# Optimization experiments

Hardware: AMD Instinct MI355X
Metric: run time of the kernel (lower is better)

The kernel has to match this reference:

```python
import jax, jax.numpy as jnp
import numpy as np
import math

B, S, L, K, NSTEPS = 32, 128, 4096, 129, 10
PAD = K // 2  # torch: int(kernel.shape[-1]/2)


def _grouped_xcorr(x, w):
    # torch F.conv1d semantics (cross-correlation), groups = channels
    # x: [B,C,L] f32, w: [C,1,K] f32 -> [B,C,L]
    return jax.lax.conv_general_dilated(
        x, w, window_strides=(1,), padding=[(PAD, PAD)],
        dimension_numbers=('NCH', 'OIH', 'NCH'), feature_group_count=x.shape[1])


def _matched_filter(x_re, x_im, k_re, k_im):
    # complex grouped conv with conj(kernel) repeated per pulse
    wc_re = jnp.tile(k_re[None, None, :], (S, 1, 1))
    wc_im = jnp.tile(-k_im[None, None, :], (S, 1, 1))  # conj
    out_re = _grouped_xcorr(x_re, wc_re) - _grouped_xcorr(x_im, wc_im)
    out_im = _grouped_xcorr(x_re, wc_im) + _grouped_xcorr(x_im, wc_re)
    return out_re + 1j * out_im  # complex64 [B,S,L]


def _produce_rd(x, w_mag, w_phase):
    phase = jnp.arctan(w_phase)                    # [B,S]
    norm_mag = S * jax.nn.softmax(w_mag, axis=-1)  # [B,S]
    iq = (norm_mag * jnp.exp(-1j * phase))[..., None] * x
    return jnp.fft.fftshift(jnp.fft.fft(iq, axis=-2), axes=-2)


def _circular_weighted_mean(w):
    # circular weighted mean of index over last axis; returns (magnitude, index)
    N = w.shape[-1]
    ang = (2.0 * jnp.pi / N) * jnp.arange(N, dtype=w.dtype)
    z = jnp.sum(w * jnp.exp(1j * ang), axis=-1)
    return jnp.abs(z), jnp.angle(z) / (2.0 * jnp.pi) * N


def _snr(rd):
    Bn, nfft, Ln = rd.shape
    e = jnp.abs(rd) ** 2                                   # [B,S,L]
    flat_idx = jnp.argmax(e.reshape(Bn, -1), axis=1)
    max_range = flat_idx % Ln                              # [B] (indices: constant wrt grad)
    col = jnp.take_along_axis(e, max_range[:, None, None], axis=2)[..., 0]  # [B,S]
    _, peak_idx = _circular_weighted_mean(col)
    # torch rounds + casts to int -> detached index
    idx = jax.lax.stop_gradient(jnp.round(peak_idx)).astype(jnp.int32) % nfft
    peak = jnp.take_along_axis(col, idx[:, None], axis=1)[:, 0]
    noise = (jnp.sum(col, axis=-1) - peak) / (nfft - 1)
    return 10.0 * jnp.log10(peak) - 10.0 * jnp.log10(noise)


def setup_inputs() -> dict:
    key = jax.random.key(0)
    ks = jax.random.split(key, 5)
    return {
        'x_re': jax.random.normal(ks[0], (B, S, L), jnp.float32),
        'x_im': jax.random.normal(ks[1], (B, S, L), jnp.float32),
        'kernel_re': jax.random.normal(ks[2], (K,), jnp.float32),
        'kernel_im': jax.random.normal(ks[3], (K,), jnp.float32),
        'log_step_mag': -2.0 * jnp.ones((S, NSTEPS), jnp.float32),
        'log_step_phase': -2.0 * jnp.ones((S, NSTEPS), jnp.float32),
        'w_phase_init': jax.random.uniform(ks[4], (B, S), jnp.float32),
    }


def reference(x_re, x_im, kernel_re, kernel_im, log_step_mag, log_step_phase, w_phase_init):
    x = _matched_filter(x_re, x_im, kernel_re, kernel_im)  # [B,S,L] complex64
    w_mag = jnp.ones((B, S), jnp.float32)
    w_phase = w_phase_init

    def loss_sum(wm, wp):
        return jnp.sum(_snr(_produce_rd(x, wm, wp)))

    grad_fn = jax.grad(loss_sum, argnums=(0, 1))
    ln10 = math.log(10.0)
    for i in range(NSTEPS):
        # torch detaches w_mag/w_phase before the inner autograd.grad
        g_mag, g_phase = grad_fn(jax.lax.stop_gradient(w_mag),
                                 jax.lax.stop_gradient(w_phase))
        lr_mag = jnp.exp(log_step_mag[:, i] * ln10)    # 10**log_step
        lr_phase = jnp.exp(log_step_phase[:, i] * ln10)
        w_mag = w_mag + lr_mag * g_mag
        w_phase = w_phase + lr_phase * g_phase
    return jnp.mean(_snr(_produce_rd(x, w_mag, w_phase)))
```

## Files before the change

kernel.cpp:

```cpp
#include <hip/hip_runtime.h>

#define BB 32
#define SS 128
#define LL 4096
#define KK 129
#define NST 10

typedef float v2f __attribute__((ext_vector_type(2)));

constexpr double PI_D = 3.141592653589793238462643383279502884;
constexpr double red_sin(double x){
  double x2 = x*x, t = x, r = x;
  t *= -x2/6.0;   r += t;
  t *= -x2/20.0;  r += t;
  t *= -x2/42.0;  r += t;
  t *= -x2/72.0;  r += t;
  t *= -x2/110.0; r += t;
  t *= -x2/156.0; r += t;
  t *= -x2/210.0; r += t;
  t *= -x2/272.0; r += t;
  return r;
}
constexpr double csin_d(double x){
  while (x >  PI_D) x -= 2.0*PI_D;
  while (x < -PI_D) x += 2.0*PI_D;
  if (x >  PI_D*0.5)      x =  PI_D - x;
  else if (x < -PI_D*0.5) x = -PI_D - x;
  return red_sin(x);
}
constexpr double ccos_d(double x){ return csin_d(x + PI_D*0.5); }
struct TWT { float c[64]; float s[64]; };
constexpr TWT make_tw(){
  TWT t{};
  for (int j = 0; j < 64; j++){
    double a = -2.0*PI_D*(double)j/128.0;
    t.c[j] = (float)ccos_d(a);
    t.s[j] = (float)csin_d(a);
  }
  return t;
}
constexpr TWT TW = make_tw();

#define PHYS8(i) ((i) + ((i) >> 3))

__device__ __forceinline__ void cfma_pk(v2f& acc, v2f xv, v2f w){
  asm("v_pk_fma_f32 %0, %1, %2, %0 op_sel:[0,0,0] op_sel_hi:[1,0,1]"
      : "+v"(acc) : "v"(xv), "v"(w));
  asm("v_pk_fma_f32 %0, %1, %2, %0 op_sel:[1,1,0] op_sel_hi:[0,1,1] neg_hi:[1,0,0]"
      : "+v"(acc) : "v"(xv), "v"(w));
}

__global__ __launch_bounds__(256) void mf_kernel(const float* __restrict__ xr,
                                                 const float* __restrict__ xi,
                                                 const float* __restrict__ kr,
                                                 const float* __restrict__ ki,
                                                 float2* __restrict__ out)
{
  const int row = blockIdx.x >> 1;
  const int l0  = (blockIdx.x & 1) * 2048;
  const int t   = threadIdx.x;
  __shared__ float2 xs[2456];

  const float* xrr = xr + (size_t)row*LL;
  const float* xir = xi + (size_t)row*LL;
  for (int i4 = t; i4 < 544; i4 += 256){
    const int g0 = l0 - 64 + i4*4;
    float4 a, c;
    if (g0 >= 0 && g0 + 3 < LL){
      a = *(const float4*)(xrr + g0);
      c = *(const float4*)(xir + g0);
    } else {
      float av[4], cv[4];
      #pragma unroll
      for (int e = 0; e < 4; ++e){
        const int g = g0 + e;
        const bool ok = (g >= 0 && g < LL);
        av[e] = ok ? xrr[g] : 0.0f;
        cv[e] = ok ? xir[g] : 0.0f;
      }
      a = make_float4(av[0],av[1],av[2],av[3]);
      c = make_float4(cv[0],cv[1],cv[2],cv[3]);
    }
    const int i = i4*4;
    const int p = PHYS8(i);
    xs[p]   = make_float2(a.x, c.x);
    xs[p+1] = make_float2(a.y, c.y);
    xs[p+2] = make_float2(a.z, c.z);
    xs[p+3] = make_float2(a.w, c.w);
  }
  __syncthreads();

  const int base_l = t*8;
  v2f ring[16];
  #pragma unroll
  for (int v = 0; v < 12; v += 2){
    const float4 p = *(const float4*)(&xs[PHYS8(base_l + v)]);
    ring[v]   = (v2f){p.x, p.y};
    ring[v+1] = (v2f){p.z, p.w};
  }

  v2f acc[8];
  #pragma unroll
  for (int j = 0; j < 8; j++) acc[j] = (v2f){0.0f, 0.0f};

  #pragma unroll 1
  for (int q8 = 0; q8 < 8; ++q8){
    #pragma unroll
    for (int qq = 0; qq < 4; ++qq){
      const int q = q8*4 + qq;
      float4 p0, p1;
      const bool doref = (q < 31);
      if (doref){
        const int v0 = base_l + q*4 + 12;
        p0 = *(const float4*)(&xs[PHYS8(v0)]);
        p1 = *(const float4*)(&xs[PHYS8(v0 + 2)]);
      }
      #pragma unroll
      for (int kk = 0; kk < 4; ++kk){
        const v2f w = (v2f){ kr[q*4 + kk], ki[q*4 + kk] };
        #pragma unroll
        for (int j = 0; j < 8; ++j){
          const int sl = (qq*4 + kk + j) & 15;
          cfma_pk(acc[j], ring[sl], w);
        }
      }
      if (doref){
        const int s0 = (qq*4 + 12) & 15;
        ring[s0]   = (v2f){p0.x, p0.y};
        ring[s0+1] = (v2f){p0.z, p0.w};
        ring[s0+2] = (v2f){p1.x, p1.y};
        ring[s0+3] = (v2f){p1.z, p1.w};
      }
    }
  }
  {
    const v2f w = (v2f){ kr[128], ki[128] };
    #pragma unroll
    for (int j = 0; j < 8; ++j) cfma_pk(acc[j], ring[j], w);
  }

  float4* orow = (float4*)(out + (size_t)row*LL + l0 + base_l);
  #pragma unroll
  for (int q = 0; q < 4; ++q){
    orow[q] = make_float4(acc[2*q][0], acc[2*q][1], acc[2*q+1][0], acc[2*q+1][1]);
  }
}

__global__ void init_kernel(const float* __restrict__ wpi,
                            float* __restrict__ w_mag, float* __restrict__ w_phase,
                            float2* __restrict__ cvec, unsigned long long* __restrict__ slots,
                            float* __restrict__ out)
{
  const int i = blockIdx.x*256 + threadIdx.x;
  if (i < BB*SS){
    float wp = wpi[i];
    w_mag[i] = 1.0f;
    w_phase[i] = wp;
    float phi = atanf(wp);
    float s, c;
    sincosf(phi, &s, &c);
    cvec[i] = make_float2(c, -s);
  }
  if (i < BB) slots[i] = 0ull;
  if (i == 0) out[0] = 0.0f;
}

template<int SPAN, int N>
__device__ __forceinline__ void fstage(float2* v){
  #pragma unroll
  for (int b0 = 0; b0 < N; b0 += 2*SPAN){
    #pragma unroll
    for (int j = 0; j < SPAN; j++){
      const int i0 = b0 + j, i1 = b0 + j + SPAN;
      float ax = v[i0].x, ay = v[i0].y, bx = v[i1].x, by = v[i1].y;
      float sx = ax - bx, sy = ay - by;
      v[i0].x = ax + bx; v[i0].y = ay + by;
      const int tj = j * (64 / SPAN);
      if (tj == 0){
        v[i1].x = sx; v[i1].y = sy;
      } else if (tj == 32){
        v[i1].x = sy; v[i1].y = -sx;
      } else {
        const float wr = TW.c[tj], wi = TW.s[tj];
        v[i1].x = sx*wr - sy*wi;
        v[i1].y = sy*wr + sx*wi;
      }
    }
  }
}

__device__ __forceinline__ void scan_fft_tail(float2* v, int r, int tid, int l,
                                              unsigned long long* wred, int nwave,
                                              unsigned long long* slot)
{
  {
    const bool hi = (r & 2) != 0;
    const float sgn = hi ? -1.0f : 1.0f;
    const bool odd = (r & 1) != 0;
    #pragma unroll
    for (int j = 0; j < 32; ++j){
      float px = __shfl_xor(v[j].x, 2);
      float py = __shfl_xor(v[j].y, 2);
      float ux = fmaf(sgn, v[j].x, px);
      float uy = fmaf(sgn, v[j].y, py);
      float wr = hi ? (odd ? TW.s[j] : TW.c[j]) : 1.0f;
      float wi = hi ? (odd ? -TW.c[j] : TW.s[j]) : 0.0f;
      v[j].x = ux*wr - uy*wi;
      v[j].y = uy*wr + ux*wi;
    }
  }
  {
    const bool hi = (r & 1) != 0;
    const float sgn = hi ? -1.0f : 1.0f;
    #pragma unroll
    for (int j = 0; j < 32; ++j){
      float px = __shfl_xor(v[j].x, 1);
      float py = __shfl_xor(v[j].y, 1);
      float ux = fmaf(sgn, v[j].x, px);
      float uy = fmaf(sgn, v[j].y, py);
      float wr = hi ? TW.c[2*j] : 1.0f;
      float wi = hi ? TW.s[2*j] : 0.0f;
      v[j].x = ux*wr - uy*wi;
      v[j].y = uy*wr + ux*wi;
    }
  }
  fstage<16,32>(v); fstage<8,32>(v); fstage<4,32>(v); fstage<2,32>(v); fstage<1,32>(v);

  float mm = 0.0f;
  #pragma unroll
  for (int j = 0; j < 32; ++j) mm = fmaxf(mm, v[j].x*v[j].x + v[j].y*v[j].y);
  mm = fmaxf(mm, __shfl_xor(mm, 1));
  mm = fmaxf(mm, __shfl_xor(mm, 2));

  unsigned long long pk = ((unsigned long long)__float_as_uint(mm) << 32) | (unsigned int)l;
  #pragma unroll
  for (int m = 4; m < 64; m <<= 1){
    unsigned long long o = __shfl_xor(pk, m);
    if (o > pk) pk = o;
  }
  if ((tid & 63) == 0) wred[tid >> 6] = pk;
  __syncthreads();
  if (tid == 0){
    unsigned long long best = wred[0];
    for (int w = 1; w < nwave; ++w) if (wred[w] > best) best = wred[w];
    atomicMax(slot, best);
  }
}

__global__ __launch_bounds__(256) void tr_scan_kernel(const float2* __restrict__ xmf,
                                                      float4* __restrict__ xt2,
                                                      const float2* __restrict__ cvec,
                                                      unsigned long long* __restrict__ slots)
{
  const int b = blockIdx.y;
  const int l0 = blockIdx.x * 64;
  const int tid = threadIdx.x;
  __shared__ float ldr[SS][65];
  __shared__ float ldi[SS][65];
  __shared__ float2 csh[SS];
  __shared__ unsigned long long wred[4];
  if (tid < SS) csh[tid] = cvec[b*SS + tid];

  #pragma unroll
  for (int it = 0; it < 16; ++it){
    const int flat = it*256 + tid;
    const int s  = flat >> 5;
    const int c4 = flat & 31;
    const float4 p = *(const float4*)(xmf + ((size_t)(b*SS + s))*LL + l0 + 2*c4);
    const int sw = 8*(s >> 5);
    ldr[s][(2*c4   + sw) & 63] = p.x;  ldi[s][(2*c4   + sw) & 63] = p.y;
    ldr[s][(2*c4+1 + sw) & 63] = p.z;  ldi[s][(2*c4+1 + sw) & 63] = p.w;
  }
  __syncthreads();

  float4* dst = xt2 + ((size_t)(b*256 + blockIdx.x*4) * 16) * 64;
  #pragma unroll
  for (int it = 0; it < 16; ++it){
    const int flat = it*256 + tid;
    const int lane = flat & 63;
    const int i   = (flat >> 6) & 15;
    const int lgl = flat >> 10;
    const int fl = lane >> 2, rr = lane & 3;
    const int lrow = lgl*16 + fl;
    const int s0 = rr*32 + 2*i;
    const int col = (lrow + 8*rr) & 63;
    dst[flat] = make_float4(ldr[s0][col], ldi[s0][col], ldr[s0+1][col], ldi[s0+1][col]);
  }

  const int f = tid >> 2, r = tid & 3;
  const int l = l0 + f;
  float2 v[32];
  #pragma unroll
  for (int j = 0; j < 32; ++j){
    const int rowi = r*32 + j;
    const int col = (f + 8*r) & 63;
    const float2 x = make_float2(ldr[rowi][col], ldi[rowi][col]);
    const float2 c = csh[rowi];
    v[j].x = c.x*x.x - c.y*x.y;
    v[j].y = c.x*x.y + c.y*x.x;
  }
  scan_fft_tail(v, r, tid, l, wred, 4, slots + b);
}

__global__ __launch_bounds__(256) void scan_t_kernel(const float4* __restrict__ xt2,
                                                     const float2* __restrict__ cvec,
                                                     unsigned long long* __restrict__ slots)
{
  const int b = blockIdx.y;
  const int tid = threadIdx.x;
  const int f = tid >> 2, r = tid & 3;
  const int l = blockIdx.x*64 + f;
  const int w = tid >> 6;
  const int lg = blockIdx.x*4 + w;
  __shared__ float2 csh[SS];
  __shared__ unsigned long long wred[4];
  if (tid < SS) csh[tid] = cvec[b*SS + tid];
  __syncthreads();

  const float4* base = xt2 + ((size_t)(b*(LL/16) + lg) * 16) * 64 + (tid & 63);
  float2 v[32];
  #pragma unroll
  for (int i = 0; i < 16; ++i){
    const float4 p = base[i*64];
    v[2*i]   = make_float2(p.x, p.y);
    v[2*i+1] = make_float2(p.z, p.w);
  }
  #pragma unroll
  for (int j = 0; j < 32; ++j){
    const float2 c = csh[r*32 + j];
    const float2 x = v[j];
    v[j].x = c.x*x.x - c.y*x.y;
    v[j].y = c.x*x.y + c.y*x.x;
  }
  scan_fft_tail(v, r, tid, l, wred, 4, slots + b);
}

__global__ __launch_bounds__(512, 4) void scan_o_kernel(const float2* __restrict__ xmf,
                                                        const float2* __restrict__ cvec,
                                                        unsigned long long* __restrict__ slots)
{
  const int b = blockIdx.y;
  const int tid = threadIdx.x;
  const int l0 = blockIdx.x * 128;
  __shared__ float2 csh[SS];
  __shared__ float2 xsh[64][130];
  __shared__ unsigned long long wred[8];
  if (tid < SS) csh[tid] = cvec[b*SS + tid];

  const int f = tid >> 2, r = tid & 3;
  float2 v[32];

  #pragma unroll 1
  for (int h = 0; h < 2; ++h){
    __syncthreads();
    const float2* src = xmf + ((size_t)(b*SS + h*64))*LL + l0;
    #pragma unroll
    for (int it = 0; it < 8; ++it){
      const int flat = it*512 + tid;
      const int s1 = flat >> 6;
      const int c4 = flat & 63;
      const float4 vv = *(const float4*)(src + (size_t)s1*LL + c4*2);
      *(float4*)(&xsh[s1][c4*2]) = vv;
    }
    __syncthreads();
    if ((r >> 1) == h){
      #pragma unroll
      for (int j = 0; j < 32; ++j){
        const int rowi = (r & 1)*32 + j;
        const float2 x = xsh[rowi][f];
        const float2 c = csh[r*32 + j];
        v[j].x = c.x*x.x - c.y*x.y;
        v[j].y = c.x*x.y + c.y*x.x;
      }
    }
  }
  scan_fft_tail(v, r, tid, l0 + f, wred, 8, slots + b);
}

__device__ __forceinline__ float wredsum(float v){
  #pragma unroll
  for (int m = 1; m < 64; m <<= 1) v += __shfl_xor(v, m);
  return v;
}
__device__ __forceinline__ float wredmax(float v){
  #pragma unroll
  for (int m = 1; m < 64; m <<= 1) v = fmaxf(v, __shfl_xor(v, m));
  return v;
}
__device__ __forceinline__ float bsum256(float v, float* red4, int t){
  v = wredsum(v);
  __syncthreads();
  if ((t & 63) == 0) red4[t >> 6] = v;
  __syncthreads();
  return red4[0] + red4[1] + red4[2] + red4[3];
}
__device__ __forceinline__ float bmax256(float v, float* red4, int t){
  v = wredmax(v);
  __syncthreads();
  if ((t & 63) == 0) red4[t >> 6] = v;
  __syncthreads();
  return fmaxf(fmaxf(red4[0], red4[1]), fmaxf(red4[2], red4[3]));
}

__global__ __launch_bounds__(256) void step_kernel(const float2* __restrict__ xmf,
                                                   float* __restrict__ w_mag,
                                                   float* __restrict__ w_phase,
                                                   float2* __restrict__ cvec,
                                                   unsigned long long* __restrict__ slots,
                                                   const float* __restrict__ lsm,
                                                   const float* __restrict__ lsp,
                                                   int stepi, int isFinal,
                                                   float* __restrict__ out)
{
  const int b = blockIdx.x, t = threadIdx.x;
  const int s = t >> 1, h = t & 1;
  __shared__ float2 ysh[SS];
  __shared__ float twc[SS], tws[SS];
  __shared__ float red4[4];
  __shared__ float speak;
  __shared__ int sidx;

  const int rbin = (int)(slots[b] & 0xffffffffull);
  const float wm0 = w_mag[b*SS + s];
  const float wp0 = w_phase[b*SS + s];
  const float2 xc = xmf[((size_t)(b*SS + s))*LL + rbin];
  float phi = atanf(wp0);
  float sph, cph;
  sincosf(phi, &sph, &cph);
  {
    int id = t & 127;
    float sv, cv;
    sincosf((float)(2.0*PI_D/128.0) * (float)id, &sv, &cv);
    twc[id] = cv; tws[id] = -sv;
  }
  float mx = bmax256(wm0, red4, t);
  float ex = expf(wm0 - mx);
  float sm = bsum256(ex, red4, t) * 0.5f;
  float m = 128.0f * ex / sm;
  float cre = m*cph, cim = -m*sph;
  ysh[s] = make_float2(cre*xc.x - cim*xc.y, cre*xc.y + cim*xc.x);
  __syncthreads();

  const int k = s;
  float Fr = 0.0f, Fi = 0.0f;
  #pragma unroll 8
  for (int q = 0; q < 64; ++q){
    int s2 = h*64 + q;
    int id = (k*s2) & 127;
    float wr = twc[id], wi = tws[id];
    float2 ys = ysh[s2];
    Fr += wr*ys.x - wi*ys.y;
    Fi += wr*ys.y + wi*ys.x;
  }
  Fr += __shfl_xor(Fr, 1);
  Fi += __shfl_xor(Fi, 1);
  const int u = (k + 64) & 127;
  float colu = Fr*Fr + Fi*Fi;

  float total = bsum256(colu, red4, t) * 0.5f;
  float zre = bsum256(colu * twc[u], red4, t) * 0.5f;
  float zim = bsum256(colu * (-tws[u]), red4, t) * 0.5f;
  if (t == 0){
    float ang = atan2f(zim, zre);
    float pidx = ang * (128.0f/(2.0f*(float)PI_D));
    sidx = ((int)rintf(pidx)) & 127;
  }
  __syncthreads();
  const int idx = sidx;
  if (u == idx && h == 0) speak = colu;
  __syncthreads();
  const float peak = speak;
  const float noise = (total - peak) * (1.0f/127.0f);

  if (isFinal){
    if (t == 0) atomicAdd(out, 10.0f*(log10f(peak) - log10f(noise)) * (1.0f/(float)BB));
    return;
  }

  constexpr float C10 = 4.342944819032518f;
  float g = (u == idx) ? (C10/peak) : (-C10/(127.0f*noise));
  __syncthreads();
  ysh[k] = make_float2(2.0f*g*Fr, 2.0f*g*Fi);
  __syncthreads();

  float Tr = 0.0f, Ti = 0.0f;
  #pragma unroll 8
  for (int q = 0; q < 64; ++q){
    int kk = h*64 + q;
    int id = (s*kk) & 127;
    float wr = twc[id], wi = -tws[id];
    float2 G = ysh[kk];
    Tr += wr*G.x - wi*G.y;
    Ti += wr*G.y + wi*G.x;
  }
  Tr += __shfl_xor(Tr, 1);
  Ti += __shfl_xor(Ti, 1);

  float Hr = xc.x*Tr + xc.y*Ti;
  float Hi = xc.x*Ti - xc.y*Tr;
  float dm   = Hr*cph - Hi*sph;
  float dphi = -m*(Hr*sph + Hi*cph);
  float S1 = bsum256(m*dm, red4, t) * 0.5f;
  float gwm = m*(dm - S1*(1.0f/128.0f));
  float gwp = dphi / (1.0f + wp0*wp0);

  constexpr float LN10 = 2.302585092994046f;
  float lrm = expf(lsm[s*NST + stepi] * LN10);
  float lrp = expf(lsp[s*NST + stepi] * LN10);
  float wm1 = wm0 + lrm*gwm;
  float wp1 = wp0 + lrp*gwp;
  if (h == 0){
    w_mag[b*SS + s] = wm1;
    w_phase[b*SS + s] = wp1;
  }

  float mx2 = bmax256(wm1, red4, t);
  float ex2 = expf(wm1 - mx2);
  float sm2 = bsum256(ex2, red4, t) * 0.5f;
  float m2 = 128.0f * ex2 / sm2;
  float phi2 = atanf(wp1);
  float s2v, c2v;
  sincosf(phi2, &s2v, &c2v);
  if (h == 0) cvec[b*SS + s] = make_float2(m2*c2v, -m2*s2v);
  if (t == 0) slots[b] = 0ull;
}

extern "C" void kernel_launch(void* const* d_in, const int* in_sizes, int n_in,
                              void* d_out, int out_size, void* d_ws, size_t ws_size,
                              hipStream_t stream)
{
  const float* x_re = (const float*)d_in[0];
  const float* x_im = (const float*)d_in[1];
  const float* k_re = (const float*)d_in[2];
  const float* k_im = (const float*)d_in[3];
  const float* lsm  = (const float*)d_in[4];
  const float* lsp  = (const float*)d_in[5];
  const float* wpi  = (const float*)d_in[6];
  float* out = (float*)d_out;

  char* ws = (char*)d_ws;
  size_t off = 0;
  float2* xmf = (float2*)(ws + off);                 off += (size_t)BB*SS*LL*sizeof(float2);
  unsigned long long* slots = (unsigned long long*)(ws + off); off += 256;
  float* w_mag   = (float*)(ws + off);               off += (size_t)BB*SS*4;
  float* w_phase = (float*)(ws + off);               off += (size_t)BB*SS*4;
  float2* cvec   = (float2*)(ws + off);              off += (size_t)BB*SS*8;
  const size_t off_base = off;
  float4* xt2 = (float4*)(ws + off);                 off += (size_t)BB*SS*LL*sizeof(float2);
  const int useT = (ws_size >= off) ? 1 : 0;
  if (ws_size < off_base) return;

  mf_kernel<<<BB*SS*2, 256, 0, stream>>>(x_re, x_im, k_re, k_im, xmf);
  init_kernel<<<(BB*SS + 255)/256, 256, 0, stream>>>(wpi, w_mag, w_phase, cvec, slots, out);

  if (useT){
    tr_scan_kernel<<<dim3(LL/64, BB), 256, 0, stream>>>(xmf, xt2, cvec, slots);
    step_kernel<<<BB, 256, 0, stream>>>(xmf, w_mag, w_phase, cvec, slots, lsm, lsp, 0, 0, out);
    for (int i = 1; i < NST; i++){
      scan_t_kernel<<<dim3(LL/64, BB), 256, 0, stream>>>(xt2, cvec, slots);
      step_kernel<<<BB, 256, 0, stream>>>(xmf, w_mag, w_phase, cvec, slots, lsm, lsp, i, 0, out);
    }
    scan_t_kernel<<<dim3(LL/64, BB), 256, 0, stream>>>(xt2, cvec, slots);
    step_kernel<<<BB, 256, 0, stream>>>(xmf, w_mag, w_phase, cvec, slots, lsm, lsp, 0, 1, out);
  } else {
    for (int i = 0; i < NST; i++){
      scan_o_kernel<<<dim3(LL/128, BB), 512, 0, stream>>>(xmf, cvec, slots);
      step_kernel<<<BB, 256, 0, stream>>>(xmf, w_mag, w_phase, cvec, slots, lsm, lsp, i, 0, out);
    }
    scan_o_kernel<<<dim3(LL/128, BB), 512, 0, stream>>>(xmf, cvec, slots);
    step_kernel<<<BB, 256, 0, stream>>>(xmf, w_mag, w_phase, cvec, slots, lsm, lsp, 0, 1, out);
  }
}
```

Before: 774.9 us.

## Compute 16 outputs per thread in matched filter and fuse step reductions

```diff
diff --git a/kernel.cpp b/kernel.cpp
--- a/kernel.cpp
+++ b/kernel.cpp
@@ -41,7 +41,8 @@
 }
 constexpr TWT TW = make_tw();
 
-#define PHYS8(i) ((i) + ((i) >> 3))
+#define PHYS8(i)  ((i) + ((i) >> 3))
+#define PHYS16(i) ((i) + ((i) >> 4))
 
 __device__ __forceinline__ void cfma_pk(v2f& acc, v2f xv, v2f w){
   asm("v_pk_fma_f32 %0, %1, %2, %0 op_sel:[0,0,0] op_sel_hi:[1,0,1]"
@@ -56,15 +57,14 @@
                                                  const float* __restrict__ ki,
                                                  float2* __restrict__ out)
 {
-  const int row = blockIdx.x >> 1;
-  const int l0  = (blockIdx.x & 1) * 2048;
+  const int row = blockIdx.x;
   const int t   = threadIdx.x;
-  __shared__ float2 xs[2456];
+  __shared__ float2 xs[4488];
 
   const float* xrr = xr + (size_t)row*LL;
   const float* xir = xi + (size_t)row*LL;
-  for (int i4 = t; i4 < 544; i4 += 256){
-    const int g0 = l0 - 64 + i4*4;
+  for (int i4 = t; i4 < 1056; i4 += 256){
+    const int g0 = i4*4 - 64;
     float4 a, c;
     if (g0 >= 0 && g0 + 3 < LL){
       a = *(const float4*)(xrr + g0);
@@ -81,8 +81,7 @@
       a = make_float4(av[0],av[1],av[2],av[3]);
       c = make_float4(cv[0],cv[1],cv[2],cv[3]);
     }
-    const int i = i4*4;
-    const int p = PHYS8(i);
+    const int p = PHYS16(i4*4);
     xs[p]   = make_float2(a.x, c.x);
     xs[p+1] = make_float2(a.y, c.y);
     xs[p+2] = make_float2(a.z, c.z);
@@ -90,58 +89,61 @@
   }
   __syncthreads();
 
-  const int base_l = t*8;
-  v2f ring[16];
-  #pragma unroll
-  for (int v = 0; v < 12; v += 2){
-    const float4 p = *(const float4*)(&xs[PHYS8(base_l + v)]);
+  const int base_l = t*16;
+  v2f ring[32];
+  #pragma unroll
+  for (int v = 0; v < 28; v += 2){
+    const float4 p = *(const float4*)(&xs[PHYS16(base_l + v)]);
     ring[v]   = (v2f){p.x, p.y};
     ring[v+1] = (v2f){p.z, p.w};
   }
 
-  v2f acc[8];
-  #pragma unroll
-  for (int j = 0; j < 8; j++) acc[j] = (v2f){0.0f, 0.0f};
+  v2f acc[16];
+  #pragma unroll
+  for (int j = 0; j < 16; j++) acc[j] = (v2f){0.0f, 0.0f};
 
   #pragma unroll 1
-  for (int q8 = 0; q8 < 8; ++q8){
+  for (int q16 = 0; q16 < 4; ++q16){
     #pragma unroll
-    for (int qq = 0; qq < 4; ++qq){
-      const int q = q8*4 + qq;
-      float4 p0, p1;
-      const bool doref = (q < 31);
-      if (doref){
-        const int v0 = base_l + q*4 + 12;
-        p0 = *(const float4*)(&xs[PHYS8(v0)]);
-        p1 = *(const float4*)(&xs[PHYS8(v0 + 2)]);
-      }
+    for (int qh = 0; qh < 2; ++qh){
       #pragma unroll
-      for (int kk = 0; kk < 4; ++kk){
-        const v2f w = (v2f){ kr[q*4 + kk], ki[q*4 + kk] };
+      for (int qq = 0; qq < 4; ++qq){
+        const int q = q16*8 + qh*4 + qq;
+        float4 p0, p1;
+        const bool doref = (q < 29);
+        if (doref){
+          const int v0 = base_l + q*4 + 28;
+          p0 = *(const float4*)(&xs[PHYS16(v0)]);
+          p1 = *(const float4*)(&xs[PHYS16(v0 + 2)]);
+        }
         #pragma unroll
-        for (int j = 0; j < 8; ++j){
-          const int sl = (qq*4 + kk + j) & 15;
-          cfma_pk(acc[j], ring[sl], w);
+        for (int kk = 0; kk < 4; ++kk){
+          const v2f w = (v2f){ kr[q*4 + kk], ki[q*4 + kk] };
+          #pragma unroll
+          for (int j = 0; j < 16; ++j){
+            const int sl = (qh*16 + qq*4 + kk + j) & 31;
+            cfma_pk(acc[j], ring[sl], w);
+          }
         }
-      }
-      if (doref){
-        const int s0 = (qq*4 + 12) & 15;
-        ring[s0]   = (v2f){p0.x, p0.y};
-        ring[s0+1] = (v2f){p0.z, p0.w};
-        ring[s0+2] = (v2f){p1.x, p1.y};
-        ring[s0+3] = (v2f){p1.z, p1.w};
+        if (doref){
+          const int s0 = (qh*16 + qq*4 + 28) & 31;
+          ring[s0]   = (v2f){p0.x, p0.y};
+          ring[s0+1] = (v2f){p0.z, p0.w};
+          ring[s0+2] = (v2f){p1.x, p1.y};
+          ring[s0+3] = (v2f){p1.z, p1.w};
+        }
       }
     }
   }
   {
     const v2f w = (v2f){ kr[128], ki[128] };
     #pragma unroll
-    for (int j = 0; j < 8; ++j) cfma_pk(acc[j], ring[j], w);
-  }
-
-  float4* orow = (float4*)(out + (size_t)row*LL + l0 + base_l);
-  #pragma unroll
-  for (int q = 0; q < 4; ++q){
+    for (int j = 0; j < 16; ++j) cfma_pk(acc[j], ring[j], w);
+  }
+
+  float4* orow = (float4*)(out + (size_t)row*LL + base_l);
+  #pragma unroll
+  for (int q = 0; q < 8; ++q){
     orow[q] = make_float4(acc[2*q][0], acc[2*q][1], acc[2*q+1][0], acc[2*q+1][1]);
   }
 }
@@ -387,19 +389,38 @@
   for (int m = 1; m < 64; m <<= 1) v = fmaxf(v, __shfl_xor(v, m));
   return v;
 }
-__device__ __forceinline__ float bsum256(float v, float* red4, int t){
+__device__ __forceinline__ float bsum256(float v, float* red, int t){
   v = wredsum(v);
   __syncthreads();
-  if ((t & 63) == 0) red4[t >> 6] = v;
-  __syncthreads();
-  return red4[0] + red4[1] + red4[2] + red4[3];
-}
-__device__ __forceinline__ float bmax256(float v, float* red4, int t){
+  if ((t & 63) == 0) red[t >> 6] = v;
+  __syncthreads();
+  return red[0] + red[1] + red[2] + red[3];
+}
+__device__ __forceinline__ float bmax256(float v, float* red, int t){
   v = wredmax(v);
   __syncthreads();
-  if ((t & 63) == 0) red4[t >> 6] = v;
-  __syncthreads();
-  return fmaxf(fmaxf(red4[0], red4[1]), fmaxf(red4[2], red4[3]));
+  if ((t & 63) == 0) red[t >> 6] = v;
+  __syncthreads();
+  return fmaxf(fmaxf(red[0], red[1]), fmaxf(red[2], red[3]));
+}
+__device__ __forceinline__ void bsum3_256(float a0, float a1, float a2,
+                                          float* red12, int t,
+                                          float& s0, float& s1, float& s2){
+  #pragma unroll
+  for (int m = 1; m < 64; m <<= 1){
+    a0 += __shfl_xor(a0, m);
+    a1 += __shfl_xor(a1, m);
+    a2 += __shfl_xor(a2, m);
+  }
+  __syncthreads();
+  if ((t & 63) == 0){
+    const int w = t >> 6;
+    red12[w] = a0; red12[w+4] = a1; red12[w+8] = a2;
+  }
+  __syncthreads();
+  s0 = red12[0]+red12[1]+red12[2]+red12[3];
+  s1 = red12[4]+red12[5]+red12[6]+red12[7];
+  s2 = red12[8]+red12[9]+red12[10]+red12[11];
 }
 
 __global__ __launch_bounds__(256) void step_kernel(const float2* __restrict__ xmf,
@@ -416,7 +437,7 @@
   const int s = t >> 1, h = t & 1;
   __shared__ float2 ysh[SS];
   __shared__ float twc[SS], tws[SS];
-  __shared__ float red4[4];
+  __shared__ float red12[12];
   __shared__ float speak;
   __shared__ int sidx;
 
@@ -428,14 +449,15 @@
   float sph, cph;
   sincosf(phi, &sph, &cph);
   {
-    int id = t & 127;
-    float sv, cv;
-    sincosf((float)(2.0*PI_D/128.0) * (float)id, &sv, &cv);
-    twc[id] = cv; tws[id] = -sv;
-  }
-  float mx = bmax256(wm0, red4, t);
+    const int id = t & 127;
+    const int lo = id & 63;
+    const float sgn2 = (id < 64) ? 1.0f : -1.0f;
+    twc[id] = sgn2 * TW.c[lo];
+    tws[id] = sgn2 * TW.s[lo];
+  }
+  float mx = bmax256(wm0, red12, t);
   float ex = expf(wm0 - mx);
-  float sm = bsum256(ex, red4, t) * 0.5f;
+  float sm = bsum256(ex, red12, t) * 0.5f;
   float m = 128.0f * ex / sm;
   float cre = m*cph, cim = -m*sph;
   ysh[s] = make_float2(cre*xc.x - cim*xc.y, cre*xc.y + cim*xc.x);
@@ -457,9 +479,9 @@
   const int u = (k + 64) & 127;
   float colu = Fr*Fr + Fi*Fi;
 
-  float total = bsum256(colu, red4, t) * 0.5f;
-  float zre = bsum256(colu * twc[u], red4, t) * 0.5f;
-  float zim = bsum256(colu * (-tws[u]), red4, t) * 0.5f;
+  float total, zre, zim;
+  bsum3_256(colu, colu * twc[u], colu * (-tws[u]), red12, t, total, zre, zim);
+  total *= 0.5f; zre *= 0.5f; zim *= 0.5f;
   if (t == 0){
     float ang = atan2f(zim, zre);
     float pidx = ang * (128.0f/(2.0f*(float)PI_D));
@@ -500,7 +522,7 @@
   float Hi = xc.x*Ti - xc.y*Tr;
   float dm   = Hr*cph - Hi*sph;
   float dphi = -m*(Hr*sph + Hi*cph);
-  float S1 = bsum256(m*dm, red4, t) * 0.5f;
+  float S1 = bsum256(m*dm, red12, t) * 0.5f;
   float gwm = m*(dm - S1*(1.0f/128.0f));
   float gwp = dphi / (1.0f + wp0*wp0);
 
@@ -514,9 +536,9 @@
     w_phase[b*SS + s] = wp1;
   }
 
-  float mx2 = bmax256(wm1, red4, t);
+  float mx2 = bmax256(wm1, red12, t);
   float ex2 = expf(wm1 - mx2);
-  float sm2 = bsum256(ex2, red4, t) * 0.5f;
+  float sm2 = bsum256(ex2, red12, t) * 0.5f;
   float m2 = 128.0f * ex2 / sm2;
   float phi2 = atanf(wp1);
   float s2v, c2v;
@@ -550,7 +572,7 @@
   const int useT = (ws_size >= off) ? 1 : 0;
   if (ws_size < off_base) return;
 
-  mf_kernel<<<BB*SS*2, 256, 0, stream>>>(x_re, x_im, k_re, k_im, xmf);
+  mf_kernel<<<BB*SS, 256, 0, stream>>>(x_re, x_im, k_re, k_im, xmf);
   init_kernel<<<(BB*SS + 255)/256, 256, 0, stream>>>(wpi, w_mag, w_phase, cvec, slots, out);
 
   if (useT){
```

Measured after the change: 759.1 us. -2.0%, faster.
